# Kernel optimization log

Hardware: AMD Instinct MI355X
Metric: run time of the kernel (lower is better)

Reference implementation:

```python
import jax, jax.numpy as jnp
import numpy as np

HIDDEN = 256


def _lstm_cell(x, h, c, W_ih, W_hh, b_ih, b_hh):
    # torch.nn.LSTMCell: gates ordered [i, f, g, o], gates = x W_ih^T + h W_hh^T + b_ih + b_hh
    gates = x @ W_ih.T + h @ W_hh.T + (b_ih + b_hh)
    i, f, g, o = jnp.split(gates, 4, axis=-1)
    c_new = jax.nn.sigmoid(f) * c + jax.nn.sigmoid(i) * jnp.tanh(g)
    h_new = jax.nn.sigmoid(o) * jnp.tanh(c_new)
    return h_new, c_new


def setup_inputs() -> dict:
    key = jax.random.key(0)
    ks = jax.random.split(key, 16)
    s = 1.0 / np.sqrt(HIDDEN)  # torch LSTMCell init scale
    inp = {
        "tracks": jax.random.normal(ks[0], (256, 512, 2), dtype=jnp.float32),
        "W_ih0": jax.random.uniform(ks[1], (1024, 2), jnp.float32, -s, s),
        "W_hh0": jax.random.uniform(ks[2], (1024, 256), jnp.float32, -s, s),
        "b_ih0": jax.random.uniform(ks[3], (1024,), jnp.float32, -s, s),
        "b_hh0": jax.random.uniform(ks[4], (1024,), jnp.float32, -s, s),
        "W_ih1": jax.random.uniform(ks[5], (1024, 256), jnp.float32, -s, s),
        "W_hh1": jax.random.uniform(ks[6], (1024, 256), jnp.float32, -s, s),
        "b_ih1": jax.random.uniform(ks[7], (1024,), jnp.float32, -s, s),
        "b_hh1": jax.random.uniform(ks[8], (1024,), jnp.float32, -s, s),
        "W_ih2": jax.random.uniform(ks[9], (1024, 256), jnp.float32, -s, s),
        "W_hh2": jax.random.uniform(ks[10], (1024, 256), jnp.float32, -s, s),
        "b_ih2": jax.random.uniform(ks[11], (1024,), jnp.float32, -s, s),
        "b_hh2": jax.random.uniform(ks[12], (1024,), jnp.float32, -s, s),
        "W_pred": jax.random.uniform(ks[13], (2, 256), jnp.float32, -s, s),
        "b_pred": jax.random.uniform(ks[14], (2,), jnp.float32, -s, s),
    }
    return inp


def reference(tracks, W_ih0, W_hh0, b_ih0, b_hh0, W_ih1, W_hh1, b_ih1, b_hh1,
              W_ih2, W_hh2, b_ih2, b_hh2, W_pred, b_pred):
    B = tracks.shape[0]
    layers = [(W_ih0, W_hh0, b_ih0, b_hh0),
              (W_ih1, W_hh1, b_ih1, b_hh1),
              (W_ih2, W_hh2, b_ih2, b_hh2)]
    zeros = jnp.zeros((B, HIDDEN), dtype=tracks.dtype)
    init_carry = tuple((zeros, zeros) for _ in layers)

    def step(carry, x_t):
        new_carry = []
        h = x_t
        for (hc, params) in zip(carry, layers):
            h, c = _lstm_cell(h, hc[0], hc[1], *params)
            new_carry.append((h, c))
        return tuple(new_carry), None

    xs = jnp.swapaxes(tracks, 0, 1)  # [T, B, 2]
    final_carry, _ = jax.lax.scan(step, init_carry, xs)
    h = final_carry[-1][0]  # last layer's final hidden state
    h = jax.nn.elu(h)
    return h @ W_pred.T + b_pred
```

## Files before the change

kernel.cpp:

```cpp
#include <hip/hip_runtime.h>
#include <math.h>

typedef __attribute__((ext_vector_type(4))) float f32x4;
typedef __attribute__((ext_vector_type(4))) int   i32x4;
typedef __attribute__((ext_vector_type(8))) short bfrag8;

#define WRE_LO_OFF 2621440
#define HB_OFF     5242880
#define FLAGS_OFF  6029312

#define WROW 264
#define SMEM_BYTES (4 * 64 * WROW * 2)

__device__ __forceinline__ unsigned short f2bf(float f){
  union { float f; unsigned u; } x; x.f = f;
  unsigned r = x.u + 0x7FFFu + ((x.u >> 16) & 1u);
  return (unsigned short)(r >> 16);
}
__device__ __forceinline__ float bf2f(unsigned short s){
  union { unsigned u; float f; } x; x.u = ((unsigned)s) << 16; return x.f;
}
__device__ __forceinline__ float sigf(float x){
  return 1.0f / (1.0f + __expf(-x));
}
__device__ __forceinline__ float tanh_fast(float x){
  x = fminf(fmaxf(x, -15.0f), 15.0f);
  float e = __expf(2.0f * x);
  return (e - 1.0f) / (e + 1.0f);
}

__device__ __forceinline__ i32x4 llc_load_b128(const void* p){
  i32x4 r;
  asm volatile("global_load_dwordx4 %0, %1, off sc0 sc1"
               : "=v"(r) : "v"(p) : "memory");
  return r;
}
__device__ __forceinline__ void llc_store_b16(void* p, unsigned short v){
  unsigned int vv = v;
  asm volatile("global_store_short %0, %1, off sc0 sc1"
               : : "v"(p), "v"(vv) : "memory");
}
__device__ __forceinline__ void wait_vm0(){
  asm volatile("s_waitcnt vmcnt(0)" ::: "memory");
}

__global__ void init_reorder(const float* __restrict__ hh0, const float* __restrict__ ih1,
                             const float* __restrict__ hh1, const float* __restrict__ ih2,
                             const float* __restrict__ hh2,
                             unsigned short* __restrict__ wre_hi,
                             unsigned short* __restrict__ wre_lo){
  int e = blockIdx.x * 256 + threadIdx.x;
  int mat = e >> 18;
  int d   = (e >> 8) & 1023;
  int k   = e & 255;
  int nt = d >> 6, g = (d >> 4) & 3, n = d & 15;
  int src_row = g*256 + nt*16 + n;
  const float* W = (mat==0) ? hh0 : (mat==1) ? ih1 : (mat==2) ? hh1 : (mat==3) ? ih2 : hh2;
  float v = W[src_row*256 + k];
  unsigned short hi = f2bf(v);
  float lo = v - bf2f(hi);
  wre_hi[e] = hi;
  wre_lo[e] = f2bf(lo);
}

__global__ void init_zero(uint4* __restrict__ p, int n16){
  int i = blockIdx.x * 256 + threadIdx.x;
  if (i < n16) p[i] = make_uint4(0u,0u,0u,0u);
}

__global__ void lstm_coop(
    const float* __restrict__ tracks,
    const float* __restrict__ wih0,
    const float* __restrict__ bih0, const float* __restrict__ bhh0,
    const float* __restrict__ bih1, const float* __restrict__ bhh1,
    const float* __restrict__ bih2, const float* __restrict__ bhh2,
    const unsigned short* __restrict__ wre_hi, const unsigned short* __restrict__ wre_lo,
    unsigned short* __restrict__ hb, unsigned int* __restrict__ flags)
{
  extern __shared__ __align__(16) unsigned short smem[];

  const int tid  = threadIdx.x;
  const int l    = blockIdx.x >> 6;
  const int r6   = blockIdx.x & 63;
  const int nt   = r6 & 15, bt = r6 >> 4;
  const int b0   = bt * 64, n0 = nt * 16;
  const int w    = tid >> 6, lane = tid & 63;
  const int m    = lane & 15, q = lane >> 4;

  unsigned int* colflags = flags + bt * 1024;
  unsigned int* mycnt    = colflags + nt * 64;

  const int nmats = (l == 0) ? 1 : 2;
  const int gmat0 = (l == 0) ? 0 : (l == 1 ? 1 : 3);
  for (int mi = 0; mi < nmats; ++mi){
    const unsigned short* sh = wre_hi + (gmat0 + mi)*262144 + nt*16384;
    const unsigned short* sl = wre_lo + (gmat0 + mi)*262144 + nt*16384;
    unsigned short* dh = smem + (mi*2 + 0)*64*WROW;
    unsigned short* dl = smem + (mi*2 + 1)*64*WROW;
    for (int c = tid; c < 2048; c += 256){
      int r = c >> 5, off = (c & 31) * 8;
      *(uint4*)(dh + r*WROW + off) = *(const uint4*)(sh + r*256 + off);
      *(uint4*)(dl + r*WROW + off) = *(const uint4*)(sl + r*256 + off);
    }
  }
  __syncthreads();

  const float* bihL = (l==0) ? bih0 : (l==1) ? bih1 : bih2;
  const float* bhhL = (l==0) ? bhh0 : (l==1) ? bhh1 : bhh2;
  float bsum[4], wx[4][2];
  #pragma unroll
  for (int g = 0; g < 4; ++g){
    int row = g*256 + n0 + m;
    bsum[g] = bihL[row] + bhhL[row];
    wx[g][0] = wih0[row*2 + 0];
    wx[g][1] = wih0[row*2 + 1];
  }
  float cst[4] = {0.f, 0.f, 0.f, 0.f};
  const int arow = b0 + 16*w + m;
  const int woff = m*WROW + q*8;

  for (int s = 0; s < 514; ++s){
    const int t = s - l;
    const bool active = (t >= 0) && (t < 512);

    float xv0[4], xv1[4];
    if (l == 0 && active){
      #pragma unroll
      for (int r = 0; r < 4; ++r){
        const float* px = tracks + (b0 + 16*w + q*4 + r)*1024 + t*2;
        xv0[r] = px[0]; xv1[r] = px[1];
      }
    }

    if (s > 0){
      if (tid < 64){
        const unsigned int tgt = 3u * (unsigned)s;
        for (;;){
          unsigned int v = tgt;
          if (tid < 16)
            v = __hip_atomic_load(colflags + tid*64, __ATOMIC_RELAXED,
                                  __HIP_MEMORY_SCOPE_AGENT);
          if (__all((int)(v >= tgt))) break;
          __builtin_amdgcn_s_sleep(1);
        }
      }
      __syncthreads();
    }

    if (active){
      const int pt = t & 1, pp = pt ^ 1;

      i32x4 ar_raw[8], ai_raw[8];
      {
        const unsigned short* prec = hb + ((pp*3 + l)*256 + arow)*256 + q*8;
        #pragma unroll
        for (int ks = 0; ks < 8; ++ks)
          ar_raw[ks] = llc_load_b128(prec + ks*32);
        if (l >= 1){
          const unsigned short* pin = hb + ((pt*3 + (l-1))*256 + arow)*256 + q*8;
          #pragma unroll
          for (int ks = 0; ks < 8; ++ks)
            ai_raw[ks] = llc_load_b128(pin + ks*32);
        }
      }
      wait_vm0();

      f32x4 acc[4];
      #pragma unroll
      for (int g = 0; g < 4; ++g) acc[g] = (f32x4){0.f,0.f,0.f,0.f};

      {
        const unsigned short* bh = smem + ((l==0?0:2) + 0)*64*WROW + woff;
        const unsigned short* bl = smem + ((l==0?0:2) + 1)*64*WROW + woff;
        #pragma unroll
        for (int ks = 0; ks < 8; ++ks){
          bfrag8 a = __builtin_bit_cast(bfrag8, ar_raw[ks]);
          #pragma unroll
          for (int g = 0; g < 4; ++g){
            bfrag8 fh = *(const bfrag8*)(bh + g*16*WROW + ks*32);
            bfrag8 fl = *(const bfrag8*)(bl + g*16*WROW + ks*32);
            acc[g] = __builtin_amdgcn_mfma_f32_16x16x32_bf16(a, fh, acc[g], 0, 0, 0);
            acc[g] = __builtin_amdgcn_mfma_f32_16x16x32_bf16(a, fl, acc[g], 0, 0, 0);
          }
        }
      }
      if (l >= 1){
        const unsigned short* bh = smem + 0*64*WROW + woff;
        const unsigned short* bl = smem + 1*64*WROW + woff;
        #pragma unroll
        for (int ks = 0; ks < 8; ++ks){
          bfrag8 a = __builtin_bit_cast(bfrag8, ai_raw[ks]);
          #pragma unroll
          for (int g = 0; g < 4; ++g){
            bfrag8 fh = *(const bfrag8*)(bh + g*16*WROW + ks*32);
            bfrag8 fl = *(const bfrag8*)(bl + g*16*WROW + ks*32);
            acc[g] = __builtin_amdgcn_mfma_f32_16x16x32_bf16(a, fh, acc[g], 0, 0, 0);
            acc[g] = __builtin_amdgcn_mfma_f32_16x16x32_bf16(a, fl, acc[g], 0, 0, 0);
          }
        }
      }

      unsigned short* hout = hb + ((pt*3 + l)*256 + 0)*256;
      #pragma unroll
      for (int r = 0; r < 4; ++r){
        float xi = 0.f, xf = 0.f, xg = 0.f, xo = 0.f;
        if (l == 0){
          xi = xv0[r]*wx[0][0] + xv1[r]*wx[0][1];
          xf = xv0[r]*wx[1][0] + xv1[r]*wx[1][1];
          xg = xv0[r]*wx[2][0] + xv1[r]*wx[2][1];
          xo = xv0[r]*wx[3][0] + xv1[r]*wx[3][1];
        }
        float gi = acc[0][r] + bsum[0] + xi;
        float gf = acc[1][r] + bsum[1] + xf;
        float gg = acc[2][r] + bsum[2] + xg;
        float go = acc[3][r] + bsum[3] + xo;
        float iv = sigf(gi);
        float fv = sigf(gf);
        float gv = tanh_fast(gg);
        float ov = sigf(go);
        cst[r] = fv * cst[r] + iv * gv;
        float hv = ov * tanh_fast(cst[r]);
        llc_store_b16(&hout[(b0 + 16*w + q*4 + r)*256 + n0 + m], f2bf(hv));
      }
    }

    wait_vm0();
    __syncthreads();
    if (tid == 0)
      __hip_atomic_fetch_add(mycnt, 1u, __ATOMIC_RELAXED, __HIP_MEMORY_SCOPE_AGENT);
  }
}

__global__ void head_kernel(const unsigned short* __restrict__ hb,
                            const float* __restrict__ wpred,
                            const float* __restrict__ bpred,
                            float* __restrict__ out){
  const int b = blockIdx.x;
  const int k = threadIdx.x;
  const int idx = (5*256 + b)*256 + k;
  float h = bf2f(hb[idx]);
  float e = (h > 0.f) ? h : expm1f(h);
  float v0 = e * wpred[k];
  float v1 = e * wpred[256 + k];
  #pragma unroll
  for (int off = 32; off > 0; off >>= 1){
    v0 += __shfl_down(v0, off, 64);
    v1 += __shfl_down(v1, off, 64);
  }
  __shared__ float r0[4], r1[4];
  int wv = threadIdx.x >> 6, ln = threadIdx.x & 63;
  if (ln == 0){ r0[wv] = v0; r1[wv] = v1; }
  __syncthreads();
  if (threadIdx.x == 0){
    out[b*2 + 0] = r0[0] + r0[1] + r0[2] + r0[3] + bpred[0];
    out[b*2 + 1] = r1[0] + r1[1] + r1[2] + r1[3] + bpred[1];
  }
}

extern "C" void kernel_launch(void* const* d_in, const int* in_sizes, int n_in,
                              void* d_out, int out_size, void* d_ws, size_t ws_size,
                              hipStream_t stream) {
  const float* tracks = (const float*)d_in[0];
  const float* wih0   = (const float*)d_in[1];
  const float* whh0   = (const float*)d_in[2];
  const float* bih0   = (const float*)d_in[3];
  const float* bhh0   = (const float*)d_in[4];
  const float* wih1   = (const float*)d_in[5];
  const float* whh1   = (const float*)d_in[6];
  const float* bih1   = (const float*)d_in[7];
  const float* bhh1   = (const float*)d_in[8];
  const float* wih2   = (const float*)d_in[9];
  const float* whh2   = (const float*)d_in[10];
  const float* bih2   = (const float*)d_in[11];
  const float* bhh2   = (const float*)d_in[12];
  const float* wpred  = (const float*)d_in[13];
  const float* bpred  = (const float*)d_in[14];
  float* out = (float*)d_out;

  char* ws = (char*)d_ws;
  unsigned short* wre_hi = (unsigned short*)(ws);
  unsigned short* wre_lo = (unsigned short*)(ws + WRE_LO_OFF);
  unsigned short* hb     = (unsigned short*)(ws + HB_OFF);
  unsigned int*   flags  = (unsigned int*)(ws + FLAGS_OFF);

  (void)hipFuncSetAttribute((const void*)lstm_coop,
                            hipFuncAttributeMaxDynamicSharedMemorySize, SMEM_BYTES);

  init_reorder<<<5120, 256, 0, stream>>>(whh0, wih1, whh1, wih2, whh2, wre_hi, wre_lo);
  init_zero<<<197, 256, 0, stream>>>((uint4*)(ws + HB_OFF), 50176);

  void* args[12];
  args[0]  = (void*)&tracks;
  args[1]  = (void*)&wih0;
  args[2]  = (void*)&bih0;
  args[3]  = (void*)&bhh0;
  args[4]  = (void*)&bih1;
  args[5]  = (void*)&bhh1;
  args[6]  = (void*)&bih2;
  args[7]  = (void*)&bhh2;
  args[8]  = (void*)&wre_hi;
  args[9]  = (void*)&wre_lo;
  args[10] = (void*)&hb;
  args[11] = (void*)&flags;
  hipLaunchCooperativeKernel((const void*)lstm_coop, dim3(192), dim3(256), args,
                             SMEM_BYTES, stream);

  head_kernel<<<256, 256, 0, stream>>>(hb, wpred, bpred, out);
}
```

Measured before the change: 3.390 ms.

## Replace global atomic counters with per-block LLC flags and targeted dependency polling

Swaps the shared per-column atomic counter, which every layer incremented and every block waited on, for per-block 'A' (inputs read) and 'F' (output written) flags stored with plain LLC-coherent stores. Each block now polls only what it depends on: the same layer's F flags, the previous layer's F flags, and the next layer's A flags so it does not overwrite buffers still being read. This is meant to remove the full cross-layer barrier each step and shorten the critical path of the wavefront. The poll loop has a guard that breaks out after a fixed count, which could hide ordering bugs. The extra __syncthreads after the loads also adds intra-block synchronisation.

```diff
diff --git a/kernel.cpp b/kernel.cpp
--- a/kernel.cpp
+++ b/kernel.cpp
@@ -7,7 +7,9 @@
 
 #define WRE_LO_OFF 2621440
 #define HB_OFF     5242880
-#define FLAGS_OFF  6029312
+#define FA_OFF     6029312
+#define FF_OFF     6078464
+#define WS_END     6127616
 
 #define WROW 264
 #define SMEM_BYTES (4 * 64 * WROW * 2)
@@ -39,6 +41,16 @@
   unsigned int vv = v;
   asm volatile("global_store_short %0, %1, off sc0 sc1"
                : : "v"(p), "v"(vv) : "memory");
+}
+__device__ __forceinline__ void llc_store_u32(void* p, unsigned v){
+  asm volatile("global_store_dword %0, %1, off sc0 sc1"
+               : : "v"(p), "v"(v) : "memory");
+}
+__device__ __forceinline__ unsigned poll_llc(const unsigned int* p){
+  unsigned r;
+  asm volatile("global_load_dword %0, %1, off sc0 sc1\n\ts_waitcnt vmcnt(0)"
+               : "=v"(r) : "v"(p) : "memory");
+  return r;
 }
 __device__ __forceinline__ void wait_vm0(){
   asm volatile("s_waitcnt vmcnt(0)" ::: "memory");
@@ -75,7 +87,7 @@
     const float* __restrict__ bih1, const float* __restrict__ bhh1,
     const float* __restrict__ bih2, const float* __restrict__ bhh2,
     const unsigned short* __restrict__ wre_hi, const unsigned short* __restrict__ wre_lo,
-    unsigned short* __restrict__ hb, unsigned int* __restrict__ flags)
+    char* __restrict__ wsb)
 {
   extern __shared__ __align__(16) unsigned short smem[];
 
@@ -87,8 +99,16 @@
   const int w    = tid >> 6, lane = tid & 63;
   const int m    = lane & 15, q = lane >> 4;
 
-  unsigned int* colflags = flags + bt * 1024;
-  unsigned int* mycnt    = colflags + nt * 64;
+  unsigned short* hb = (unsigned short*)(wsb + HB_OFF);
+
+  unsigned* FAb = (unsigned*)(wsb + FA_OFF) + bt*(3*16*64);
+  unsigned* FFb = (unsigned*)(wsb + FF_OFF) + bt*(3*16*64);
+  unsigned* myA = FAb + (l*16 + nt)*64;
+  unsigned* myF = FFb + (l*16 + nt)*64;
+  const unsigned* pollp = nullptr;
+  if (tid < 16)                                pollp = FFb + (l*16 + tid)*64;
+  else if (tid < 32 && l >= 1)                 pollp = FFb + ((l-1)*16 + (tid-16))*64;
+  else if (tid >= 32 && tid < 48 && l <= 1)    pollp = FAb + ((l+1)*16 + (tid-32))*64;
 
   const int nmats = (l == 0) ? 1 : 2;
   const int gmat0 = (l == 0) ? 0 : (l == 1 ? 1 : 3);
@@ -133,38 +153,39 @@
     }
 
     if (s > 0){
-      if (tid < 64){
-        const unsigned int tgt = 3u * (unsigned)s;
-        for (;;){
-          unsigned int v = tgt;
-          if (tid < 16)
-            v = __hip_atomic_load(colflags + tid*64, __ATOMIC_RELAXED,
-                                  __HIP_MEMORY_SCOPE_AGENT);
-          if (__all((int)(v >= tgt))) break;
+      if (tid < 64 && pollp != nullptr){
+        const unsigned tgt = (unsigned)s;
+        int guard = 0;
+        while (poll_llc(pollp) < tgt){
           __builtin_amdgcn_s_sleep(1);
+          if (++guard > 20000) break;
         }
       }
       __syncthreads();
     }
 
+    i32x4 ar_raw[8], ai_raw[8];
+    int pt = 0;
     if (active){
-      const int pt = t & 1, pp = pt ^ 1;
-
-      i32x4 ar_raw[8], ai_raw[8];
-      {
-        const unsigned short* prec = hb + ((pp*3 + l)*256 + arow)*256 + q*8;
+      pt = t & 1;
+      const int pp = pt ^ 1;
+      const unsigned short* prec = hb + ((pp*3 + l)*256 + arow)*256 + q*8;
+      #pragma unroll
+      for (int ks = 0; ks < 8; ++ks)
+        ar_raw[ks] = llc_load_b128(prec + ks*32);
+      if (l >= 1){
+        const unsigned short* pin = hb + ((pt*3 + (l-1))*256 + arow)*256 + q*8;
         #pragma unroll
         for (int ks = 0; ks < 8; ++ks)
-          ar_raw[ks] = llc_load_b128(prec + ks*32);
-        if (l >= 1){
-          const unsigned short* pin = hb + ((pt*3 + (l-1))*256 + arow)*256 + q*8;
-          #pragma unroll
-          for (int ks = 0; ks < 8; ++ks)
-            ai_raw[ks] = llc_load_b128(pin + ks*32);
-        }
+          ai_raw[ks] = llc_load_b128(pin + ks*32);
       }
       wait_vm0();
-
+      __builtin_amdgcn_sched_barrier(0);
+    }
+    __syncthreads();
+    if (tid == 0) llc_store_u32(myA, (unsigned)(s + 1));
+
+    if (active){
       f32x4 acc[4];
       #pragma unroll
       for (int g = 0; g < 4; ++g) acc[g] = (f32x4){0.f,0.f,0.f,0.f};
@@ -225,9 +246,9 @@
     }
 
     wait_vm0();
+    __builtin_amdgcn_sched_barrier(0);
     __syncthreads();
-    if (tid == 0)
-      __hip_atomic_fetch_add(mycnt, 1u, __ATOMIC_RELAXED, __HIP_MEMORY_SCOPE_AGENT);
+    if (tid == 0) llc_store_u32(myF, (unsigned)(s + 1));
   }
 }
 
@@ -277,19 +298,18 @@
   const float* bpred  = (const float*)d_in[14];
   float* out = (float*)d_out;
 
-  char* ws = (char*)d_ws;
-  unsigned short* wre_hi = (unsigned short*)(ws);
-  unsigned short* wre_lo = (unsigned short*)(ws + WRE_LO_OFF);
-  unsigned short* hb     = (unsigned short*)(ws + HB_OFF);
-  unsigned int*   flags  = (unsigned int*)(ws + FLAGS_OFF);
+  char* wsb = (char*)d_ws;
+  unsigned short* wre_hi = (unsigned short*)(wsb);
+  unsigned short* wre_lo = (unsigned short*)(wsb + WRE_LO_OFF);
+  const unsigned short* hb = (const unsigned short*)(wsb + HB_OFF);
 
   (void)hipFuncSetAttribute((const void*)lstm_coop,
                             hipFuncAttributeMaxDynamicSharedMemorySize, SMEM_BYTES);
 
   init_reorder<<<5120, 256, 0, stream>>>(whh0, wih1, whh1, wih2, whh2, wre_hi, wre_lo);
-  init_zero<<<197, 256, 0, stream>>>((uint4*)(ws + HB_OFF), 50176);
-
-  void* args[12];
+  init_zero<<<216, 256, 0, stream>>>((uint4*)(wsb + HB_OFF), 55296);
+
+  void* args[11];
   args[0]  = (void*)&tracks;
   args[1]  = (void*)&wih0;
   args[2]  = (void*)&bih0;
@@ -300,8 +320,7 @@
   args[7]  = (void*)&bhh2;
   args[8]  = (void*)&wre_hi;
   args[9]  = (void*)&wre_lo;
-  args[10] = (void*)&hb;
-  args[11] = (void*)&flags;
+  args[10] = (void*)&wsb;
   hipLaunchCooperativeKernel((const void*)lstm_coop, dim3(192), dim3(256), args,
                              SMEM_BYTES, stream);
 
```

After: 4.038 ms. 1.19x slower.
